# Kernel optimization log

Measured on AMD Instinct MI355X. Metric: run time of the kernel, lower is better.

Reference implementation:

```python
import jax, jax.numpy as jnp
import numpy as np

NEG_SLOPE = 0.2  # PyG GATConv default
BN_EPS = 1e-5
NUM_GRAPHS = 128


def _bn(x, g, b, m, v):
    # eval-mode BatchNorm1d with running stats
    return (x - m) * jax.lax.rsqrt(v + BN_EPS) * g + b


def _gat_conv(x, src, dst, mask, W, a_src, a_dst, bias):
    # PyG GATConv: per-head linear, edge logits LeakyReLU(a_src.Wx_j + a_dst.Wx_i),
    # segment-softmax over incoming edges of each dst node, scatter-add messages.
    N = x.shape[0]
    H, C = a_src.shape
    xw = (x @ W).reshape(N, H, C)                       # [N,H,C]
    logit_s = (xw * a_src).sum(-1)                      # [N,H]
    logit_d = (xw * a_dst).sum(-1)                      # [N,H]
    e = jax.nn.leaky_relu(logit_s[src] + logit_d[dst], NEG_SLOPE)  # [E,H]
    e = jnp.where(mask[:, None], e, -1e30)              # edges filtered by edge_weights==1
    m = jax.ops.segment_max(e, dst, num_segments=N)     # [N,H]
    m = jnp.maximum(m, -1e30)                           # guard empty segments
    p = jnp.exp(e - m[dst]) * mask[:, None].astype(e.dtype)
    denom = jax.ops.segment_sum(p, dst, num_segments=N) + 1e-16
    alpha = p / denom[dst]                              # [E,H]
    out = jax.ops.segment_sum(xw[src] * alpha[..., None], dst, num_segments=N)
    return out.reshape(N, H * C) + bias


def setup_inputs() -> dict:
    key = jax.random.key(0)
    ks = jax.random.split(key, 20)
    N, E, F, G, NC = 20000, 320000, 128, NUM_GRAPHS, 10
    E0, E1, H = 256, 512, 2
    C = E1 // H

    def lin(k, fi, fo):
        return jax.random.normal(k, (fi, fo), jnp.float32) / np.float32(np.sqrt(fi))

    def bn(k, n):
        k1, k2, k3, k4 = jax.random.split(k, 4)
        g = 1.0 + 0.1 * jax.random.normal(k1, (n,), jnp.float32)
        b = 0.1 * jax.random.normal(k2, (n,), jnp.float32)
        m = 0.1 * jax.random.normal(k3, (n,), jnp.float32)
        v = 1.0 + 0.5 * jax.random.uniform(k4, (n,), jnp.float32)
        return g, b, m, v

    d = {}
    d['x'] = jax.random.normal(ks[0], (N, F), jnp.float32)
    d['edge_index'] = jax.random.randint(ks[1], (2, E), 0, N, dtype=jnp.int32)
    d['edge_weights'] = jnp.ones((E,), jnp.int32)
    d['batch'] = jnp.sort(jax.random.randint(ks[2], (N,), 0, G, dtype=jnp.int32))
    d['mlp_w1'] = lin(ks[3], F, E0); d['mlp_b1'] = jnp.zeros((E0,), jnp.float32)
    d['bn1_g'], d['bn1_b'], d['bn1_m'], d['bn1_v'] = bn(ks[4], E0)
    d['mlp_w2'] = lin(ks[5], E0, E0); d['mlp_b2'] = jnp.zeros((E0,), jnp.float32)
    d['bn2_g'], d['bn2_b'], d['bn2_m'], d['bn2_v'] = bn(ks[6], E0)
    d['gat0_w'] = lin(ks[7], E0, H * C)
    d['gat0_asrc'] = 0.1 * jax.random.normal(ks[8], (H, C), jnp.float32)
    d['gat0_adst'] = 0.1 * jax.random.normal(ks[9], (H, C), jnp.float32)
    d['gat0_bias'] = jnp.zeros((H * C,), jnp.float32)
    d['gat1_w'] = lin(ks[10], E1, H * C)
    d['gat1_asrc'] = 0.1 * jax.random.normal(ks[11], (H, C), jnp.float32)
    d['gat1_adst'] = 0.1 * jax.random.normal(ks[12], (H, C), jnp.float32)
    d['gat1_bias'] = jnp.zeros((H * C,), jnp.float32)
    d['bn3_g'], d['bn3_b'], d['bn3_m'], d['bn3_v'] = bn(ks[13], E1)
    d['fin_w1'] = lin(ks[14], E1, E1); d['fin_b1'] = jnp.zeros((E1,), jnp.float32)
    d['fin_w2'] = lin(ks[15], E1, NC); d['fin_b2'] = jnp.zeros((NC,), jnp.float32)
    return d


def reference(x, edge_index, edge_weights, batch,
              mlp_w1, mlp_b1, bn1_g, bn1_b, bn1_m, bn1_v,
              mlp_w2, mlp_b2, bn2_g, bn2_b, bn2_m, bn2_v,
              gat0_w, gat0_asrc, gat0_adst, gat0_bias,
              gat1_w, gat1_asrc, gat1_adst, gat1_bias,
              bn3_g, bn3_b, bn3_m, bn3_v,
              fin_w1, fin_b1, fin_w2, fin_b2):
    src, dst = edge_index[0], edge_index[1]
    mask = edge_weights == 1
    # initial MLP (dropout is identity in eval)
    h = jax.nn.relu(_bn(x @ mlp_w1 + mlp_b1, bn1_g, bn1_b, bn1_m, bn1_v))
    h = jax.nn.relu(_bn(h @ mlp_w2 + mlp_b2, bn2_g, bn2_b, bn2_m, bn2_v))
    # GAT layers
    h = _gat_conv(h, src, dst, mask, gat0_w, gat0_asrc, gat0_adst, gat0_bias)
    h = _gat_conv(h, src, dst, mask, gat1_w, gat1_asrc, gat1_adst, gat1_bias)
    # global mean pool over graphs
    sums = jax.ops.segment_sum(h, batch, num_segments=NUM_GRAPHS)
    cnt = jax.ops.segment_sum(jnp.ones((h.shape[0], 1), h.dtype), batch, num_segments=NUM_GRAPHS)
    pooled = sums / jnp.maximum(cnt, 1.0)
    # final head: BN -> ReLU -> Linear -> ReLU -> Linear
    z = jax.nn.relu(_bn(pooled, bn3_g, bn3_b, bn3_m, bn3_v))
    z = jax.nn.relu(z @ fin_w1 + fin_b1)
    return z @ fin_w2 + fin_b2
```

## Files before the change

kernel.cpp:

```cpp
#include <hip/hip_runtime.h>

typedef unsigned short u16;

constexpr int NN = 20000;
constexpr int EE = 320000;
constexpr int FD = 128;
constexpr int C0 = 256;
constexpr int C1 = 512;
constexpr int NG = 128;
constexpr int NC = 10;
constexpr int NBLK = (NN + 255) / 256;
constexpr int HB  = 320;
constexpr int EST = HB * 256;
constexpr int LGB = 640;
constexpr int PSPL = 16;

constexpr size_t OFF_XB   = 0;
constexpr size_t OFF_H1   = OFF_XB  + (size_t)NN * FD * 2;
constexpr size_t OFF_H2   = OFF_H1  + (size_t)NN * C0 * 2;
constexpr size_t OFF_XW   = OFF_H2  + (size_t)NN * C0 * 2;
constexpr size_t OFF_H34  = OFF_XW  + (size_t)NN * C1 * 2;
constexpr size_t OFF_LS   = OFF_H34 + (size_t)NN * C1 * 2;
constexpr size_t OFF_LD   = OFF_LS  + (size_t)NN * 2 * 4;
constexpr size_t OFF_DEG  = OFF_LD  + (size_t)NN * 2 * 4;
constexpr size_t OFF_OFFS = OFF_DEG + (size_t)NN * 4;
constexpr size_t OFF_CUR  = OFF_OFFS + 80016;
constexpr size_t OFF_CSRC = OFF_CUR + (size_t)NN * 4;
constexpr size_t OFF_GCNT = OFF_CSRC + (size_t)EE * 4;
constexpr size_t OFF_GOFF = OFF_GCNT + 512;
constexpr size_t OFF_PART = OFF_GOFF + 768;
constexpr size_t OFF_PTOT = OFF_PART + 512;
constexpr size_t OFF_Z1   = OFF_PTOT + 256;
constexpr size_t OFF_Z2   = OFF_Z1  + (size_t)NG * C1 * 2;
constexpr size_t OFF_ST   = OFF_Z2  + (size_t)NG * C1 * 2;
constexpr size_t OFF_W1T  = OFF_ST  + 8192;
constexpr size_t OFF_W2T  = OFF_W1T + (size_t)FD * C0 * 2;
constexpr size_t OFF_G0T  = OFF_W2T + (size_t)C0 * C0 * 2;
constexpr size_t OFF_G1T  = OFF_G0T + (size_t)C0 * C1 * 2;
constexpr size_t OFF_AUX  = OFF_G1T + (size_t)C1 * C1 * 2;
constexpr size_t OFF_FLAG = OFF_AUX  + 0;
constexpr size_t OFF_A0S  = OFF_AUX  + 256;
constexpr size_t OFF_A0D  = OFF_AUX  + 1280;
constexpr size_t OFF_A1S  = OFF_AUX  + 2304;
constexpr size_t OFF_A1D  = OFF_AUX  + 3328;
constexpr size_t OFF_GB0  = OFF_AUX  + 4352;
constexpr size_t OFF_GB1  = OFF_AUX  + 6400;
constexpr size_t OFF_FB1  = OFF_AUX  + 8448;
constexpr size_t OFF_FB2  = OFF_AUX  + 10496;
constexpr size_t OFF_GMX  = OFF_AUX  + 10752;
constexpr size_t OFF_PP   = OFF_AUX  + 11008;
constexpr size_t OFF_P0   = OFF_XB;
constexpr size_t OFF_P1   = OFF_XB + (size_t)EE * 4;

__device__ inline float bf2f(u16 u) { return __uint_as_float(((unsigned)u) << 16); }
__device__ inline u16 f2bf(float f) {
    unsigned u = __float_as_uint(f);
    unsigned r = u + 0x7fffu + ((u >> 16) & 1u);
    return (u16)(r >> 16);
}
__device__ inline float ldf(const void* p, long i, unsigned f) {
    return f ? ((const float*)p)[i] : bf2f(((const u16*)p)[i]);
}
__device__ inline unsigned encf(float f) {
    unsigned u = __float_as_uint(f);
    return (u & 0x80000000u) ? ~u : (u | 0x80000000u);
}
__device__ inline float decf(unsigned e) {
    return (e & 0x80000000u) ? __uint_as_float(e ^ 0x80000000u) : __uint_as_float(~e);
}
__device__ inline void unpack8(uint4 r, float* v) {
    v[0] = __uint_as_float(r.x << 16); v[1] = __uint_as_float(r.x & 0xffff0000u);
    v[2] = __uint_as_float(r.y << 16); v[3] = __uint_as_float(r.y & 0xffff0000u);
    v[4] = __uint_as_float(r.z << 16); v[5] = __uint_as_float(r.z & 0xffff0000u);
    v[6] = __uint_as_float(r.w << 16); v[7] = __uint_as_float(r.w & 0xffff0000u);
}

typedef __bf16 bf16x8_t __attribute__((ext_vector_type(8)));
typedef float  f32x4_t  __attribute__((ext_vector_type(4)));

__device__ __forceinline__ void gl_lds16(const u16* g, u16* l) {
    __builtin_amdgcn_global_load_lds((const __attribute__((address_space(1))) void*)g,
                                     (__attribute__((address_space(3))) void*)l, 16, 0, 0);
}

__global__ void detect_dtype(const u16* __restrict__ x, const u16* __restrict__ w,
                             const u16* __restrict__ fw, unsigned* flag) {
    __shared__ int cnt;
    if (threadIdx.x == 0) cnt = 0;
    __syncthreads();
    int c = 0;
    for (int i = threadIdx.x; i < 4096; i += 256) {
        c += (((x[i]  >> 7) & 0xFF) == 0xFF);
        c += (((w[i]  >> 7) & 0xFF) == 0xFF);
        c += (((fw[i] >> 7) & 0xFF) == 0xFF);
    }
    atomicAdd(&cnt, c);
    __syncthreads();
    if (threadIdx.x == 0) *flag = (cnt >= 2) ? 1u : 0u;
}

__global__ void cvt_x(const unsigned* __restrict__ flag, const void* __restrict__ xin,
                      u16* __restrict__ XB, int* __restrict__ deg, int* __restrict__ gcnt,
                      unsigned* __restrict__ gmxu) {
    int i = blockIdx.x * 256 + threadIdx.x;
    if (i < NN) deg[i] = 0;
    if (i < NG) gcnt[i] = 0;
    if (i < 4)  gmxu[i] = encf(-1e30f);
    if (*flag) {
        float4 v = ((const float4*)xin)[i];
        ushort4 r;
        r.x = f2bf(v.x); r.y = f2bf(v.y); r.z = f2bf(v.z); r.w = f2bf(v.w);
        ((ushort4*)XB)[i] = r;
    } else {
        ((ushort4*)XB)[i] = ((const ushort4*)xin)[i];
    }
}

__global__ void prep_params(const unsigned* __restrict__ flag,
                            const void* g1, const void* b1, const void* m1, const void* v1, const void* lb1,
                            const void* g2, const void* b2, const void* m2, const void* v2, const void* lb2,
                            const void* g3, const void* b3, const void* m3, const void* v3,
                            const void* a0s, const void* a0d, const void* gb0in,
                            const void* a1s, const void* a1d, const void* gb1in,
                            const void* fb1in, const void* fb2in,
                            float* S1, float* T1, float* S2, float* T2, float* S3, float* T3,
                            u16* A0S, u16* A0D, u16* A1S, u16* A1D,
                            float* GB0, float* GB1, float* FB1, float* FB2) {
    unsigned f = *flag;
    int c = threadIdx.x;
    if (c < 256) {
        float s = ldf(g1, c, f) / sqrtf(ldf(v1, c, f) + 1e-5f);
        S1[c] = s; T1[c] = s * (ldf(lb1, c, f) - ldf(m1, c, f)) + ldf(b1, c, f);
        float s2 = ldf(g2, c, f) / sqrtf(ldf(v2, c, f) + 1e-5f);
        S2[c] = s2; T2[c] = s2 * (ldf(lb2, c, f) - ldf(m2, c, f)) + ldf(b2, c, f);
    }
    float s3 = ldf(g3, c, f) / sqrtf(ldf(v3, c, f) + 1e-5f);
    S3[c] = s3; T3[c] = ldf(b3, c, f) - ldf(m3, c, f) * s3;
    A0S[c] = f2bf(ldf(a0s, c, f));
    A0D[c] = f2bf(ldf(a0d, c, f));
    A1S[c] = f2bf(ldf(a1s, c, f));
    A1D[c] = f2bf(ldf(a1d, c, f));
    GB0[c] = ldf(gb0in, c, f);
    GB1[c] = ldf(gb1in, c, f);
    FB1[c] = ldf(fb1in, c, f);
    if (c < NC) FB2[c] = ldf(fb2in, c, f);
}

__global__ void transpose_all(const unsigned* __restrict__ flag,
                              const void* __restrict__ w1, const void* __restrict__ w2,
                              const void* __restrict__ g0, const void* __restrict__ g1,
                              u16* __restrict__ w1T, u16* __restrict__ w2T,
                              u16* __restrict__ g0T, u16* __restrict__ g1T) {
    int b = blockIdx.x;
    const void* B; u16* BT; int K, logN, base;
    if (b < 128)      { B = w1; BT = w1T; K = FD; logN = 8; base = 0; }
    else if (b < 384) { B = w2; BT = w2T; K = C0; logN = 8; base = 128; }
    else if (b < 896) { B = g0; BT = g0T; K = C0; logN = 9; base = 384; }
    else              { B = g1; BT = g1T; K = C1; logN = 9; base = 896; }
    int idx = (b - base) * 256 + threadIdx.x;
    int N = 1 << logN;
    int k = idx >> logN, n = idx & (N - 1);
    u16 v = (*flag) ? f2bf(((const float*)B)[idx]) : ((const u16*)B)[idx];
    BT[(size_t)n * K + k] = v;
}

__global__ __launch_bounds__(256) void hist_k(const int* __restrict__ dst, const int* __restrict__ ew,
                                              const int* __restrict__ batch,
                                              int* __restrict__ deg, int* __restrict__ gcnt) {
    int tid = blockIdx.x * 256 + threadIdx.x;
    int lane = threadIdx.x & 63;
#pragma unroll
    for (int j = 0; j < 4; j++) {
        int e = tid + j * EST;
        if (e < EE && ew[e] == 1) atomicAdd(&deg[dst[e]], 1);
    }
    int n = tid;
    if (n < NN) {
        int g = batch[n];
        int pg = __shfl_up(g, 1);
        bool head = (lane == 0) || (pg != g);
        unsigned long long act = __ballot(1);
        unsigned long long hm  = __ballot(head);
        if (head) {
            unsigned long long above = (lane < 63) ? ((hm >> (lane + 1)) << (lane + 1)) : 0ull;
            int limit = 64 - __builtin_clzll(act);
            int nxt = above ? __builtin_ctzll(above) : limit;
            atomicAdd(&gcnt[g], nxt - lane);
        }
    }
}
__global__ __launch_bounds__(256) void scan_blk(const int* __restrict__ deg, int* __restrict__ off,
                                                int* __restrict__ part) {
    __shared__ int tmp[256];
    int tid = threadIdx.x, i = blockIdx.x * 256 + tid;
    int v = (i < NN) ? deg[i] : 0;
    tmp[tid] = v;
    __syncthreads();
#pragma unroll
    for (int s = 1; s < 256; s <<= 1) {
        int a = (tid >= s) ? tmp[tid - s] : 0;
        __syncthreads();
        if (tid >= s) tmp[tid] += a;
        __syncthreads();
    }
    if (i < NN) off[i] = tmp[tid] - v;
    if (tid == 255) part[blockIdx.x] = tmp[255];
}
__global__ __launch_bounds__(128) void scan_small(int* __restrict__ part, int* __restrict__ ptot,
                                                  const int* __restrict__ gcnt, int* __restrict__ goff) {
    __shared__ int tmp[128];
    int tid = threadIdx.x;
    int v = (tid < NBLK) ? part[tid] : 0;
    tmp[tid] = v;
    __syncthreads();
#pragma unroll
    for (int s = 1; s < 128; s <<= 1) {
        int a = (tid >= s) ? tmp[tid - s] : 0;
        __syncthreads();
        if (tid >= s) tmp[tid] += a;
        __syncthreads();
    }
    if (tid < NBLK) part[tid] = tmp[tid] - v;
    if (tid == 127) *ptot = tmp[127];
    __syncthreads();
    int g = gcnt[tid];
    tmp[tid] = g;
    __syncthreads();
#pragma unroll
    for (int s = 1; s < 128; s <<= 1) {
        int a = (tid >= s) ? tmp[tid - s] : 0;
        __syncthreads();
        if (tid >= s) tmp[tid] += a;
        __syncthreads();
    }
    goff[tid] = tmp[tid] - g;
    if (tid == 127) goff[128] = tmp[127];
}
__global__ __launch_bounds__(256) void scan_add(int* __restrict__ off, const int* __restrict__ part,
                                                const int* __restrict__ ptot, int* __restrict__ cursor) {
    int tid = threadIdx.x, i = blockIdx.x * 256 + tid;
    if (i < NN) {
        int o = off[i] + part[blockIdx.x];
        off[i] = o;
        cursor[i] = o;
    }
    if (i == 0) off[NN] = *ptot;
}
__global__ __launch_bounds__(256) void csr_fill(const int* __restrict__ src, const int* __restrict__ dst,
                                                const int* __restrict__ ew,
                                                int* __restrict__ cursor, u16* __restrict__ csrc) {
    int tid = blockIdx.x * 256 + threadIdx.x;
    bool ok[4]; int sv[4]; int p[4];
#pragma unroll
    for (int j = 0; j < 4; j++) {
        int e = tid + j * EST;
        ok[j] = false; sv[j] = 0; p[j] = 0;
        if (e < EE && ew[e] == 1) {
            ok[j] = true;
            sv[j] = src[e];
            p[j] = atomicAdd(&cursor[dst[e]], 1);
        }
    }
#pragma unroll
    for (int j = 0; j < 4; j++) if (ok[j]) csrc[p[j]] = (u16)sv[j];
}

template <int EPI>
__global__ __launch_bounds__(256) void gemm_tile(const u16* __restrict__ A, const u16* __restrict__ BT,
                                                 u16* __restrict__ Cm,
                                                 const float* __restrict__ S, const float* __restrict__ T,
                                                 int M, int N, int K) {
    __shared__ u16 As[128 * 32];
    __shared__ u16 Bs[128 * 32];
    const int tid  = threadIdx.x;
    const int wave = tid >> 6;
    const int lane = tid & 63;
    const int quad = lane >> 4;
    const int l16  = lane & 15;
    const int wr0  = (wave >> 1) * 64;
    const int wc0  = (wave & 1) * 64;
    const int row0 = blockIdx.x * 128;
    const int col0 = blockIdx.y * 128;

    const int lr = lane >> 2;
    const int lk = (lane & 3) * 8;
    int r0l = wave * 32 + lr;
    int r1l = r0l + 16;
    int gr0 = row0 + r0l; if (gr0 >= M) gr0 = M - 1;
    int gr1 = row0 + r1l; if (gr1 >= M) gr1 = M - 1;
    const u16* ga0 = A  + (size_t)gr0 * K + lk;
    const u16* ga1 = A  + (size_t)gr1 * K + lk;
    const u16* gb0 = BT + (size_t)(col0 + r0l) * K + lk;
    const u16* gb1 = BT + (size_t)(col0 + r1l) * K + lk;
    u16* la0 = As + (size_t)(wave * 32)      * 32 + lane * 8;
    u16* la1 = As + (size_t)(wave * 32 + 16) * 32 + lane * 8;
    u16* lb0 = Bs + (size_t)(wave * 32)      * 32 + lane * 8;
    u16* lb1 = Bs + (size_t)(wave * 32 + 16) * 32 + lane * 8;

    f32x4_t acc[4][4];
#pragma unroll
    for (int r = 0; r < 4; r++)
#pragma unroll
        for (int c = 0; c < 4; c++)
#pragma unroll
            for (int i = 0; i < 4; i++) acc[r][c][i] = 0.f;

    for (int k0 = 0; k0 < K; k0 += 32) {
        gl_lds16(ga0 + k0, la0);
        gl_lds16(ga1 + k0, la1);
        gl_lds16(gb0 + k0, lb0);
        gl_lds16(gb1 + k0, lb1);
        __syncthreads();

        bf16x8_t a[4], b[4];
#pragma unroll
        for (int r = 0; r < 4; r++)
            a[r] = *(const bf16x8_t*)(As + (size_t)(wr0 + r * 16 + l16) * 32 + quad * 8);
#pragma unroll
        for (int c = 0; c < 4; c++)
            b[c] = *(const bf16x8_t*)(Bs + (size_t)(wc0 + c * 16 + l16) * 32 + quad * 8);
#pragma unroll
        for (int r = 0; r < 4; r++)
#pragma unroll
            for (int c = 0; c < 4; c++)
                acc[r][c] = __builtin_amdgcn_mfma_f32_16x16x32_bf16(a[r], b[c], acc[r][c], 0, 0, 0);
        __syncthreads();
    }

#pragma unroll
    for (int r = 0; r < 4; r++) {
        int rb = row0 + wr0 + r * 16 + quad * 4;
#pragma unroll
        for (int c = 0; c < 4; c++) {
            int col = col0 + wc0 + c * 16 + l16;
            float sc = (EPI == 1) ? S[col] : 0.f;
            float sh = (EPI == 1) ? T[col] : 0.f;
#pragma unroll
            for (int i = 0; i < 4; i++) {
                int row = rb + i;
                if (row < M) {
                    float v = acc[r][c][i];
                    if (EPI == 1) v = fmaxf(v * sc + sh, 0.f);
                    Cm[(size_t)row * N + col] = f2bf(v);
                }
            }
        }
    }
}

__global__ __launch_bounds__(256) void gat_logits(const u16* __restrict__ xw, const u16* __restrict__ asrc,
                                                  const u16* __restrict__ adst, float* __restrict__ ls,
                                                  float* __restrict__ ld, unsigned* __restrict__ gmx) {
    __shared__ float smax[8];
    int lane = threadIdx.x & 63;
    int wv   = threadIdx.x >> 6;
    int h    = lane >> 5;
    uint4 av = ((const uint4*)asrc)[lane];
    uint4 dv = ((const uint4*)adst)[lane];
    float a[8], d[8];
    unpack8(av, a); unpack8(dv, d);
    float mm = -1e30f;
    int n = blockIdx.x * 4 + wv;
    uint4 xv;
    if (n < NN) xv = ((const uint4*)(xw + (size_t)n * C1))[lane];
    while (n < NN) {
        int n2 = n + LGB * 4;
        uint4 nx;
        if (n2 < NN) nx = ((const uint4*)(xw + (size_t)n2 * C1))[lane];
        float x[8];
        unpack8(xv, x);
        float ps = 0.f, pd = 0.f;
#pragma unroll
        for (int j = 0; j < 8; j++) { ps += x[j] * a[j]; pd += x[j] * d[j]; }
#pragma unroll
        for (int m = 16; m >= 1; m >>= 1) { ps += __shfl_xor(ps, m); pd += __shfl_xor(pd, m); }
        if ((lane & 31) == 0) {
            ls[n * 2 + h] = ps;
            ld[n * 2 + h] = pd;
        }
        mm = fmaxf(mm, ps);
        xv = nx; n = n2;
    }
    if ((lane & 31) == 0) smax[wv * 2 + h] = mm;
    __syncthreads();
    if (threadIdx.x < 2) {
        float m = fmaxf(fmaxf(smax[threadIdx.x], smax[2 + threadIdx.x]),
                        fmaxf(smax[4 + threadIdx.x], smax[6 + threadIdx.x]));
        atomicMax(&gmx[threadIdx.x], encf(m));
    }
}

__global__ __launch_bounds__(256) void gat_prep(const int* __restrict__ off, const u16* __restrict__ csrc,
                                                const float* __restrict__ ls, const float* __restrict__ ld,
                                                const unsigned* __restrict__ gmx,
                                                float* __restrict__ P0, float* __restrict__ P1) {
    int n = blockIdx.x * 4 + (threadIdx.x >> 6);
    if (n >= NN) return;
    int lane = threadIdx.x & 63;
    int h = lane >> 5;
    int el = lane & 31;
    int beg = off[n], end = off[n + 1];
    if (beg >= end) return;
    float2 ldv = ((const float2*)ld)[n];
    float ldh = h ? ldv.y : ldv.x;
    float gm = decf(gmx[h]) + ldh;
    float mhat = gm > 0.f ? gm : 0.2f * gm;
    float* __restrict__ Ph = h ? P1 : P0;
    float den = 0.f;
    for (int base = beg; base < end; base += 32) {
        int e = base + el;
        int ec = e < end ? e : end - 1;
        int sv = csrc[ec];
        float vv = ls[sv * 2 + h] + ldh;
        vv = vv > 0.f ? vv : 0.2f * vv;
        float p = __expf(vv - mhat);
        float pm = (e < end) ? p : 0.f;
#pragma unroll
        for (int m = 16; m >= 1; m >>= 1) pm += __shfl_xor(pm, m);
        den += pm;
        if (e < end) Ph[e] = p;
    }
    float inv = 1.f / fmaxf(den, 1e-30f);
    for (int base = beg; base < end; base += 32) {
        int e = base + el;
        if (e < end) Ph[e] *= inv;
    }
}

__device__ __forceinline__ void proc_edge(uint4 c, float w, float* acc) {
    float x[8];
    unpack8(c, x);
#pragma unroll
    for (int q = 0; q < 8; q++) acc[q] = fmaf(w, x[q], acc[q]);
}

__global__ __launch_bounds__(256) void gat_aggregate(const int* __restrict__ off, const u16* __restrict__ csrc,
                                                     const float* __restrict__ P0, const float* __restrict__ P1,
                                                     const u16* __restrict__ xw,
                                                     const float* __restrict__ bias, u16* __restrict__ outh) {
    int n = blockIdx.x * 4 + (threadIdx.x >> 6);
    if (n >= NN) return;
    const int lane = threadIdx.x & 63;
    const int h    = lane >> 5;
    const int el   = lane & 31;
    const int hoff = h << 5;
    const float* __restrict__ Ph = h ? P1 : P0;
    int beg = off[n], end = off[n + 1];

    float acc[8];
#pragma unroll
    for (int q = 0; q < 8; q++) acc[q] = 0.f;

#define ROWLD(S) (((const uint4*)(xw + (size_t)(S) * C1))[lane])

    for (int base = beg; base < end; base += 32) {
        int cnt = end - base; if (cnt > 32) cnt = 32;
        int e = base + el;
        int ec = e < end ? e : end - 1;
        int sv = csrc[ec];
        float pv = Ph[ec];

        uint4 r0 = ROWLD(__shfl(sv, 0));
        uint4 r1 = ROWLD(__shfl(sv, 1));
        uint4 r2 = ROWLD(__shfl(sv, 2));
        uint4 r3 = ROWLD(__shfl(sv, 3));

        for (int j = 0; j < cnt; j += 4) {
            uint4 c0 = r0, c1 = r1, c2 = r2, c3 = r3;
            float w0 = __shfl(pv, j + hoff);
            float w1 = __shfl(pv, j + 1 + hoff);
            float w2 = __shfl(pv, j + 2 + hoff);
            float w3 = __shfl(pv, j + 3 + hoff);
            if (j + 4 < cnt) {
                r0 = ROWLD(__shfl(sv, j + 4));
                r1 = ROWLD(__shfl(sv, j + 5));
                r2 = ROWLD(__shfl(sv, j + 6));
                r3 = ROWLD(__shfl(sv, j + 7));
            }
            proc_edge(c0, w0, acc);
            if (j + 1 < cnt) proc_edge(c1, w1, acc);
            if (j + 2 < cnt) proc_edge(c2, w2, acc);
            if (j + 3 < cnt) proc_edge(c3, w3, acc);
        }
    }
#undef ROWLD

    int cb = lane * 8;
    const float4* bp = (const float4*)(bias + cb);
    float4 b0 = bp[0], b1 = bp[1];
    uint4 st;
    st.x = (unsigned)f2bf(acc[0] + b0.x) | ((unsigned)f2bf(acc[1] + b0.y) << 16);
    st.y = (unsigned)f2bf(acc[2] + b0.z) | ((unsigned)f2bf(acc[3] + b0.w) << 16);
    st.z = (unsigned)f2bf(acc[4] + b1.x) | ((unsigned)f2bf(acc[5] + b1.y) << 16);
    st.w = (unsigned)f2bf(acc[6] + b1.z) | ((unsigned)f2bf(acc[7] + b1.w) << 16);
    ((uint4*)(outh + (size_t)n * C1 + cb))[0] = st;
}

__global__ __launch_bounds__(128) void pool_part(const u16* __restrict__ h4, const int* __restrict__ goff,
                                                 float* __restrict__ pp) {
    int g = blockIdx.x, s = blockIdx.y, t = threadIdx.x;
    int b = goff[g], e = goff[g + 1];
    int len = e - b;
    int chunk = (len + PSPL - 1) / PSPL;
    int n0 = b + s * chunk;
    int n1 = n0 + chunk; if (n1 > e) n1 = e;
    float s0 = 0.f, s1 = 0.f, s2 = 0.f, s3 = 0.f;
    for (int n = n0; n < n1; n++) {
        ushort4 v = *(const ushort4*)(h4 + (size_t)n * C1 + t * 4);
        s0 += bf2f(v.x); s1 += bf2f(v.y); s2 += bf2f(v.z); s3 += bf2f(v.w);
    }
    float4* dst = (float4*)(pp + ((size_t)g * PSPL + s) * C1 + t * 4);
    *dst = make_float4(s0, s1, s2, s3);
}

__global__ __launch_bounds__(512) void pool_fin(const float* __restrict__ pp, const int* __restrict__ goff,
                                                const float* __restrict__ S3, const float* __restrict__ T3,
                                                u16* __restrict__ z1) {
    int g = blockIdx.x, t = threadIdx.x;
    float s = 0.f;
#pragma unroll
    for (int k = 0; k < PSPL; k++) s += pp[((size_t)g * PSPL + k) * C1 + t];
    int b = goff[g], e = goff[g + 1];
    float mean = s / fmaxf((float)(e - b), 1.f);
    float v = mean * S3[t] + T3[t];
    z1[(size_t)g * C1 + t] = f2bf(fmaxf(v, 0.f));
}

__global__ __launch_bounds__(512) void head_fc1(const unsigned* __restrict__ flag, const u16* __restrict__ z1,
                                                const void* __restrict__ w1, const float* __restrict__ FB1,
                                                u16* __restrict__ z2) {
    __shared__ float zrow[512];
    int g = blockIdx.x, t = threadIdx.x;
    zrow[t] = bf2f(z1[(size_t)g * 512 + t]);
    __syncthreads();
    float acc = 0.f;
    if (*flag) {
        const float* w = (const float*)w1;
        for (int k = 0; k < 512; k++) acc = fmaf(zrow[k], w[(size_t)k * 512 + t], acc);
    } else {
        const u16* w = (const u16*)w1;
        for (int k = 0; k < 512; k++) acc = fmaf(zrow[k], bf2f(w[(size_t)k * 512 + t]), acc);
    }
    acc += FB1[t];
    z2[(size_t)g * 512 + t] = f2bf(fmaxf(acc, 0.f));
}
__global__ __launch_bounds__(64) void head_fc2(const unsigned* __restrict__ flag, const u16* __restrict__ z2,
                                               const void* __restrict__ w2, const float* __restrict__ FB2,
                                               void* __restrict__ out) {
    int g = blockIdx.x, o = blockIdx.y, lane = threadIdx.x;
    unsigned f = *flag;
    float acc = 0.f;
    if (f) {
        const float* w = (const float*)w2;
        for (int k = lane; k < 512; k += 64) acc += bf2f(z2[(size_t)g * 512 + k]) * w[(size_t)k * NC + o];
    } else {
        const u16* w = (const u16*)w2;
        for (int k = lane; k < 512; k += 64) acc += bf2f(z2[(size_t)g * 512 + k]) * bf2f(w[(size_t)k * NC + o]);
    }
#pragma unroll
    for (int m = 32; m >= 1; m >>= 1) acc += __shfl_xor(acc, m);
    if (lane == 0) {
        float v = acc + FB2[o];
        if (f) ((float*)out)[g * NC + o] = v;
        else   ((u16*)out)[g * NC + o] = f2bf(v);
    }
}

extern "C" void kernel_launch(void* const* d_in, const int* in_sizes, int n_in,
                              void* d_out, int out_size, void* d_ws, size_t ws_size,
                              hipStream_t stream) {
    (void)in_sizes; (void)n_in; (void)out_size; (void)ws_size;

    const void* x      = d_in[0];
    const int* ei      = (const int*)d_in[1];
    const int* src     = ei;
    const int* dst     = ei + EE;
    const int* ew      = (const int*)d_in[2];
    const int* batch   = (const int*)d_in[3];
    const void* mlp_w1 = d_in[4];
    const void* mlp_b1 = d_in[5];
    const void *bn1g = d_in[6], *bn1b = d_in[7], *bn1m = d_in[8], *bn1v = d_in[9];
    const void* mlp_w2 = d_in[10];
    const void* mlp_b2 = d_in[11];
    const void *bn2g = d_in[12], *bn2b = d_in[13], *bn2m = d_in[14], *bn2v = d_in[15];
    const void* g0w    = d_in[16];
    const void* g0as   = d_in[17];
    const void* g0ad   = d_in[18];
    const void* g0bias = d_in[19];
    const void* g1w    = d_in[20];
    const void* g1as   = d_in[21];
    const void* g1ad   = d_in[22];
    const void* g1bias = d_in[23];
    const void *bn3g = d_in[24], *bn3b = d_in[25], *bn3m = d_in[26], *bn3v = d_in[27];
    const void* fin_w1 = d_in[28];
    const void* fin_b1 = d_in[29];
    const void* fin_w2 = d_in[30];
    const void* fin_b2 = d_in[31];

    char* ws = (char*)d_ws;
    u16*  XB   = (u16*)(ws + OFF_XB);
    u16*  h1   = (u16*)(ws + OFF_H1);
    u16*  h2   = (u16*)(ws + OFF_H2);
    u16*  xw   = (u16*)(ws + OFF_XW);
    u16*  h34  = (u16*)(ws + OFF_H34);
    float* ls  = (float*)(ws + OFF_LS);
    float* ld  = (float*)(ws + OFF_LD);
    int*  deg  = (int*)(ws + OFF_DEG);
    int*  off  = (int*)(ws + OFF_OFFS);
    int*  cur  = (int*)(ws + OFF_CUR);
    u16*  csrc = (u16*)(ws + OFF_CSRC);
    int*  gcnt = (int*)(ws + OFF_GCNT);
    int*  goff = (int*)(ws + OFF_GOFF);
    int*  part = (int*)(ws + OFF_PART);
    int*  ptot = (int*)(ws + OFF_PTOT);
    u16*  z1   = (u16*)(ws + OFF_Z1);
    u16*  z2   = (u16*)(ws + OFF_Z2);
    float* S1 = (float*)(ws + OFF_ST);
    float* T1 = S1 + 256;
    float* S2 = T1 + 256;
    float* T2 = S2 + 256;
    float* S3 = T2 + 256;
    float* T3 = S3 + 512;
    u16* w1T = (u16*)(ws + OFF_W1T);
    u16* w2T = (u16*)(ws + OFF_W2T);
    u16* g0T = (u16*)(ws + OFF_G0T);
    u16* g1T = (u16*)(ws + OFF_G1T);
    unsigned* flag = (unsigned*)(ws + OFF_FLAG);
    u16* A0S = (u16*)(ws + OFF_A0S);
    u16* A0D = (u16*)(ws + OFF_A0D);
    u16* A1S = (u16*)(ws + OFF_A1S);
    u16* A1D = (u16*)(ws + OFF_A1D);
    float* GB0 = (float*)(ws + OFF_GB0);
    float* GB1 = (float*)(ws + OFF_GB1);
    float* FB1 = (float*)(ws + OFF_FB1);
    float* FB2 = (float*)(ws + OFF_FB2);
    unsigned* GMXU = (unsigned*)(ws + OFF_GMX);
    float* PP = (float*)(ws + OFF_PP);
    float* P0 = (float*)(ws + OFF_P0);
    float* P1 = (float*)(ws + OFF_P1);

    detect_dtype<<<1, 256, 0, stream>>>((const u16*)x, (const u16*)mlp_w1, (const u16*)fin_w1, flag);
    cvt_x<<<(NN * FD / 4) / 256, 256, 0, stream>>>(flag, x, XB, deg, gcnt, GMXU);
    prep_params<<<1, 512, 0, stream>>>(flag,
                                       bn1g, bn1b, bn1m, bn1v, mlp_b1,
                                       bn2g, bn2b, bn2m, bn2v, mlp_b2,
                                       bn3g, bn3b, bn3m, bn3v,
                                       g0as, g0ad, g0bias, g1as, g1ad, g1bias,
                                       fin_b1, fin_b2,
                                       S1, T1, S2, T2, S3, T3,
                                       A0S, A0D, A1S, A1D, GB0, GB1, FB1, FB2);
    transpose_all<<<1920, 256, 0, stream>>>(flag, mlp_w1, mlp_w2, g0w, g1w, w1T, w2T, g0T, g1T);

    hist_k<<<HB, 256, 0, stream>>>(dst, ew, batch, deg, gcnt);
    scan_blk<<<NBLK, 256, 0, stream>>>(deg, off, part);
    scan_small<<<1, 128, 0, stream>>>(part, ptot, gcnt, goff);
    scan_add<<<NBLK, 256, 0, stream>>>(off, part, ptot, cur);
    csr_fill<<<HB, 256, 0, stream>>>(src, dst, ew, cur, csrc);

    gemm_tile<1><<<dim3(157, 2), 256, 0, stream>>>(XB, w1T, h1, S1, T1, NN, C0, FD);
    gemm_tile<1><<<dim3(157, 2), 256, 0, stream>>>(h1, w2T, h2, S2, T2, NN, C0, C0);

    gemm_tile<0><<<dim3(157, 4), 256, 0, stream>>>(h2, g0T, xw, nullptr, nullptr, NN, C1, C0);
    gat_logits<<<LGB, 256, 0, stream>>>(xw, A0S, A0D, ls, ld, GMXU);
    gat_prep<<<NN / 4, 256, 0, stream>>>(off, csrc, ls, ld, GMXU, P0, P1);
    gat_aggregate<<<NN / 4, 256, 0, stream>>>(off, csrc, P0, P1, xw, GB0, h34);

    gemm_tile<0><<<dim3(157, 4), 256, 0, stream>>>(h34, g1T, xw, nullptr, nullptr, NN, C1, C1);
    gat_logits<<<LGB, 256, 0, stream>>>(xw, A1S, A1D, ls, ld, GMXU + 2);
    gat_prep<<<NN / 4, 256, 0, stream>>>(off, csrc, ls, ld, GMXU + 2, P0, P1);
    gat_aggregate<<<NN / 4, 256, 0, stream>>>(off, csrc, P0, P1, xw, GB1, h34);

    pool_part<<<dim3(NG, PSPL), 128, 0, stream>>>(h34, goff, PP);
    pool_fin<<<NG, 512, 0, stream>>>(PP, goff, S3, T3, z1);
    head_fc1<<<NG, 512, 0, stream>>>(flag, z1, fin_w1, FB1, z2);
    head_fc2<<<dim3(NG, NC), 64, 0, stream>>>(flag, z2, fin_w2, FB2, d_out);
}
```

Measured before the change: 407.1 us.

## Fuse param prep with transposes, defer softmax normalization, merge head kernels

Merges the parameter-prep and weight-transpose kernels into one launch, and combines pool_fin, head_fc1 and head_fc2 into a single head kernel. GAT prep no longer rescales the per-edge probabilities in a second pass. It stores each node's denominator, and the aggregate kernel multiplies its accumulator by the reciprocal in the epilogue. This removes several launches and one read-write pass over the edge weights, at the cost of an extra small buffer and a serial shared-memory reduction for the final layer.

After: 405.7 us. About the same (-0.4%).

```diff
diff --git a/kernel.cpp b/kernel.cpp
--- a/kernel.cpp
+++ b/kernel.cpp
@@ -49,6 +49,7 @@
 constexpr size_t OFF_FB2  = OFF_AUX  + 10496;
 constexpr size_t OFF_GMX  = OFF_AUX  + 10752;
 constexpr size_t OFF_PP   = OFF_AUX  + 11008;
+constexpr size_t OFF_DENA = OFF_PP + (size_t)NG * PSPL * C1 * 4;
 constexpr size_t OFF_P0   = OFF_XB;
 constexpr size_t OFF_P1   = OFF_XB + (size_t)EE * 4;
 
@@ -116,7 +117,7 @@
     }
 }
 
-__global__ void prep_params(const unsigned* __restrict__ flag,
+__global__ __launch_bounds__(512) void prep_trans(const unsigned* __restrict__ flag,
                             const void* g1, const void* b1, const void* m1, const void* v1, const void* lb1,
                             const void* g2, const void* b2, const void* m2, const void* v2, const void* lb2,
                             const void* g3, const void* b3, const void* m3, const void* v3,
@@ -125,42 +126,40 @@
                             const void* fb1in, const void* fb2in,
                             float* S1, float* T1, float* S2, float* T2, float* S3, float* T3,
                             u16* A0S, u16* A0D, u16* A1S, u16* A1D,
-                            float* GB0, float* GB1, float* FB1, float* FB2) {
+                            float* GB0, float* GB1, float* FB1, float* FB2,
+                            const void* w1, const void* w2, const void* g0w, const void* g1w,
+                            u16* w1T, u16* w2T, u16* g0T, u16* g1T) {
     unsigned f = *flag;
-    int c = threadIdx.x;
-    if (c < 256) {
-        float s = ldf(g1, c, f) / sqrtf(ldf(v1, c, f) + 1e-5f);
-        S1[c] = s; T1[c] = s * (ldf(lb1, c, f) - ldf(m1, c, f)) + ldf(b1, c, f);
-        float s2 = ldf(g2, c, f) / sqrtf(ldf(v2, c, f) + 1e-5f);
-        S2[c] = s2; T2[c] = s2 * (ldf(lb2, c, f) - ldf(m2, c, f)) + ldf(b2, c, f);
-    }
-    float s3 = ldf(g3, c, f) / sqrtf(ldf(v3, c, f) + 1e-5f);
-    S3[c] = s3; T3[c] = ldf(b3, c, f) - ldf(m3, c, f) * s3;
-    A0S[c] = f2bf(ldf(a0s, c, f));
-    A0D[c] = f2bf(ldf(a0d, c, f));
-    A1S[c] = f2bf(ldf(a1s, c, f));
-    A1D[c] = f2bf(ldf(a1d, c, f));
-    GB0[c] = ldf(gb0in, c, f);
-    GB1[c] = ldf(gb1in, c, f);
-    FB1[c] = ldf(fb1in, c, f);
-    if (c < NC) FB2[c] = ldf(fb2in, c, f);
-}
-
-__global__ void transpose_all(const unsigned* __restrict__ flag,
-                              const void* __restrict__ w1, const void* __restrict__ w2,
-                              const void* __restrict__ g0, const void* __restrict__ g1,
-                              u16* __restrict__ w1T, u16* __restrict__ w2T,
-                              u16* __restrict__ g0T, u16* __restrict__ g1T) {
-    int b = blockIdx.x;
+    if (blockIdx.x == 0) {
+        int c = threadIdx.x;
+        if (c < 256) {
+            float s = ldf(g1, c, f) / sqrtf(ldf(v1, c, f) + 1e-5f);
+            S1[c] = s; T1[c] = s * (ldf(lb1, c, f) - ldf(m1, c, f)) + ldf(b1, c, f);
+            float s2 = ldf(g2, c, f) / sqrtf(ldf(v2, c, f) + 1e-5f);
+            S2[c] = s2; T2[c] = s2 * (ldf(lb2, c, f) - ldf(m2, c, f)) + ldf(b2, c, f);
+        }
+        float s3 = ldf(g3, c, f) / sqrtf(ldf(v3, c, f) + 1e-5f);
+        S3[c] = s3; T3[c] = ldf(b3, c, f) - ldf(m3, c, f) * s3;
+        A0S[c] = f2bf(ldf(a0s, c, f));
+        A0D[c] = f2bf(ldf(a0d, c, f));
+        A1S[c] = f2bf(ldf(a1s, c, f));
+        A1D[c] = f2bf(ldf(a1d, c, f));
+        GB0[c] = ldf(gb0in, c, f);
+        GB1[c] = ldf(gb1in, c, f);
+        FB1[c] = ldf(fb1in, c, f);
+        if (c < NC) FB2[c] = ldf(fb2in, c, f);
+        return;
+    }
+    int b = blockIdx.x - 1;
     const void* B; u16* BT; int K, logN, base;
-    if (b < 128)      { B = w1; BT = w1T; K = FD; logN = 8; base = 0; }
-    else if (b < 384) { B = w2; BT = w2T; K = C0; logN = 8; base = 128; }
-    else if (b < 896) { B = g0; BT = g0T; K = C0; logN = 9; base = 384; }
-    else              { B = g1; BT = g1T; K = C1; logN = 9; base = 896; }
-    int idx = (b - base) * 256 + threadIdx.x;
+    if (b < 64)       { B = w1;  BT = w1T; K = FD; logN = 8; base = 0; }
+    else if (b < 192) { B = w2;  BT = w2T; K = C0; logN = 8; base = 64; }
+    else if (b < 448) { B = g0w; BT = g0T; K = C0; logN = 9; base = 192; }
+    else              { B = g1w; BT = g1T; K = C1; logN = 9; base = 448; }
+    int idx = (b - base) * 512 + threadIdx.x;
     int N = 1 << logN;
     int k = idx >> logN, n = idx & (N - 1);
-    u16 v = (*flag) ? f2bf(((const float*)B)[idx]) : ((const u16*)B)[idx];
+    u16 v = f ? f2bf(((const float*)B)[idx]) : ((const u16*)B)[idx];
     BT[(size_t)n * K + k] = v;
 }
 
@@ -393,14 +392,14 @@
 __global__ __launch_bounds__(256) void gat_prep(const int* __restrict__ off, const u16* __restrict__ csrc,
                                                 const float* __restrict__ ls, const float* __restrict__ ld,
                                                 const unsigned* __restrict__ gmx,
-                                                float* __restrict__ P0, float* __restrict__ P1) {
+                                                float* __restrict__ P0, float* __restrict__ P1,
+                                                float* __restrict__ denA) {
     int n = blockIdx.x * 4 + (threadIdx.x >> 6);
     if (n >= NN) return;
     int lane = threadIdx.x & 63;
     int h = lane >> 5;
     int el = lane & 31;
     int beg = off[n], end = off[n + 1];
-    if (beg >= end) return;
     float2 ldv = ((const float2*)ld)[n];
     float ldh = h ? ldv.y : ldv.x;
     float gm = decf(gmx[h]) + ldh;
@@ -420,11 +419,7 @@
         den += pm;
         if (e < end) Ph[e] = p;
     }
-    float inv = 1.f / fmaxf(den, 1e-30f);
-    for (int base = beg; base < end; base += 32) {
-        int e = base + el;
-        if (e < end) Ph[e] *= inv;
-    }
+    if (el == 0) denA[n * 2 + h] = den;
 }
 
 __device__ __forceinline__ void proc_edge(uint4 c, float w, float* acc) {
@@ -436,6 +431,7 @@
 
 __global__ __launch_bounds__(256) void gat_aggregate(const int* __restrict__ off, const u16* __restrict__ csrc,
                                                      const float* __restrict__ P0, const float* __restrict__ P1,
+                                                     const float* __restrict__ denA,
                                                      const u16* __restrict__ xw,
                                                      const float* __restrict__ bias, u16* __restrict__ outh) {
     int n = blockIdx.x * 4 + (threadIdx.x >> 6);
@@ -485,14 +481,15 @@
     }
 #undef ROWLD
 
+    float inv = 1.f / fmaxf(denA[n * 2 + h], 1e-30f);
     int cb = lane * 8;
     const float4* bp = (const float4*)(bias + cb);
     float4 b0 = bp[0], b1 = bp[1];
     uint4 st;
-    st.x = (unsigned)f2bf(acc[0] + b0.x) | ((unsigned)f2bf(acc[1] + b0.y) << 16);
-    st.y = (unsigned)f2bf(acc[2] + b0.z) | ((unsigned)f2bf(acc[3] + b0.w) << 16);
-    st.z = (unsigned)f2bf(acc[4] + b1.x) | ((unsigned)f2bf(acc[5] + b1.y) << 16);
-    st.w = (unsigned)f2bf(acc[6] + b1.z) | ((unsigned)f2bf(acc[7] + b1.w) << 16);
+    st.x = (unsigned)f2bf(fmaf(acc[0], inv, b0.x)) | ((unsigned)f2bf(fmaf(acc[1], inv, b0.y)) << 16);
+    st.y = (unsigned)f2bf(fmaf(acc[2], inv, b0.z)) | ((unsigned)f2bf(fmaf(acc[3], inv, b0.w)) << 16);
+    st.z = (unsigned)f2bf(fmaf(acc[4], inv, b1.x)) | ((unsigned)f2bf(fmaf(acc[5], inv, b1.y)) << 16);
+    st.w = (unsigned)f2bf(fmaf(acc[6], inv, b1.z)) | ((unsigned)f2bf(fmaf(acc[7], inv, b1.w)) << 16);
     ((uint4*)(outh + (size_t)n * C1 + cb))[0] = st;
 }
 
@@ -513,28 +510,27 @@
     *dst = make_float4(s0, s1, s2, s3);
 }
 
-__global__ __launch_bounds__(512) void pool_fin(const float* __restrict__ pp, const int* __restrict__ goff,
+__global__ __launch_bounds__(512) void head_all(const unsigned* __restrict__ flag,
+                                                const float* __restrict__ pp, const int* __restrict__ goff,
                                                 const float* __restrict__ S3, const float* __restrict__ T3,
-                                                u16* __restrict__ z1) {
+                                                const void* __restrict__ w1, const float* __restrict__ FB1,
+                                                const void* __restrict__ w2, const float* __restrict__ FB2,
+                                                void* __restrict__ out) {
+    __shared__ float zrow[512];
+    __shared__ float z2row[512];
+    __shared__ float red[512];
     int g = blockIdx.x, t = threadIdx.x;
+    unsigned f = *flag;
     float s = 0.f;
 #pragma unroll
     for (int k = 0; k < PSPL; k++) s += pp[((size_t)g * PSPL + k) * C1 + t];
     int b = goff[g], e = goff[g + 1];
     float mean = s / fmaxf((float)(e - b), 1.f);
-    float v = mean * S3[t] + T3[t];
-    z1[(size_t)g * C1 + t] = f2bf(fmaxf(v, 0.f));
-}
-
-__global__ __launch_bounds__(512) void head_fc1(const unsigned* __restrict__ flag, const u16* __restrict__ z1,
-                                                const void* __restrict__ w1, const float* __restrict__ FB1,
-                                                u16* __restrict__ z2) {
-    __shared__ float zrow[512];
-    int g = blockIdx.x, t = threadIdx.x;
-    zrow[t] = bf2f(z1[(size_t)g * 512 + t]);
+    float v = fmaxf(mean * S3[t] + T3[t], 0.f);
+    zrow[t] = bf2f(f2bf(v));
     __syncthreads();
     float acc = 0.f;
-    if (*flag) {
+    if (f) {
         const float* w = (const float*)w1;
         for (int k = 0; k < 512; k++) acc = fmaf(zrow[k], w[(size_t)k * 512 + t], acc);
     } else {
@@ -542,27 +538,25 @@
         for (int k = 0; k < 512; k++) acc = fmaf(zrow[k], bf2f(w[(size_t)k * 512 + t]), acc);
     }
     acc += FB1[t];
-    z2[(size_t)g * 512 + t] = f2bf(fmaxf(acc, 0.f));
-}
-__global__ __launch_bounds__(64) void head_fc2(const unsigned* __restrict__ flag, const u16* __restrict__ z2,
-                                               const void* __restrict__ w2, const float* __restrict__ FB2,
-                                               void* __restrict__ out) {
-    int g = blockIdx.x, o = blockIdx.y, lane = threadIdx.x;
-    unsigned f = *flag;
-    float acc = 0.f;
-    if (f) {
-        const float* w = (const float*)w2;
-        for (int k = lane; k < 512; k += 64) acc += bf2f(z2[(size_t)g * 512 + k]) * w[(size_t)k * NC + o];
-    } else {
-        const u16* w = (const u16*)w2;
-        for (int k = lane; k < 512; k += 64) acc += bf2f(z2[(size_t)g * 512 + k]) * bf2f(w[(size_t)k * NC + o]);
-    }
-#pragma unroll
-    for (int m = 32; m >= 1; m >>= 1) acc += __shfl_xor(acc, m);
-    if (lane == 0) {
-        float v = acc + FB2[o];
-        if (f) ((float*)out)[g * NC + o] = v;
-        else   ((u16*)out)[g * NC + o] = f2bf(v);
+    z2row[t] = bf2f(f2bf(fmaxf(acc, 0.f)));
+    __syncthreads();
+    float z2t = z2row[t];
+    for (int o = 0; o < NC; o++) {
+        float p = f ? z2t * ((const float*)w2)[(size_t)t * NC + o]
+                    : z2t * bf2f(((const u16*)w2)[(size_t)t * NC + o]);
+        red[t] = p;
+        __syncthreads();
+#pragma unroll
+        for (int sd = 256; sd >= 1; sd >>= 1) {
+            if (t < sd) red[t] += red[t + sd];
+            __syncthreads();
+        }
+        if (t == 0) {
+            float vv = red[0] + FB2[o];
+            if (f) ((float*)out)[g * NC + o] = vv;
+            else   ((u16*)out)[g * NC + o] = f2bf(vv);
+        }
+        __syncthreads();
     }
 }
 
@@ -613,8 +607,6 @@
     int*  goff = (int*)(ws + OFF_GOFF);
     int*  part = (int*)(ws + OFF_PART);
     int*  ptot = (int*)(ws + OFF_PTOT);
-    u16*  z1   = (u16*)(ws + OFF_Z1);
-    u16*  z2   = (u16*)(ws + OFF_Z2);
     float* S1 = (float*)(ws + OFF_ST);
     float* T1 = S1 + 256;
     float* S2 = T1 + 256;
@@ -636,20 +628,21 @@
     float* FB2 = (float*)(ws + OFF_FB2);
     unsigned* GMXU = (unsigned*)(ws + OFF_GMX);
     float* PP = (float*)(ws + OFF_PP);
+    float* DENA = (float*)(ws + OFF_DENA);
     float* P0 = (float*)(ws + OFF_P0);
     float* P1 = (float*)(ws + OFF_P1);
 
     detect_dtype<<<1, 256, 0, stream>>>((const u16*)x, (const u16*)mlp_w1, (const u16*)fin_w1, flag);
     cvt_x<<<(NN * FD / 4) / 256, 256, 0, stream>>>(flag, x, XB, deg, gcnt, GMXU);
-    prep_params<<<1, 512, 0, stream>>>(flag,
-                                       bn1g, bn1b, bn1m, bn1v, mlp_b1,
-                                       bn2g, bn2b, bn2m, bn2v, mlp_b2,
-                                       bn3g, bn3b, bn3m, bn3v,
-                                       g0as, g0ad, g0bias, g1as, g1ad, g1bias,
-                                       fin_b1, fin_b2,
-                                       S1, T1, S2, T2, S3, T3,
-                                       A0S, A0D, A1S, A1D, GB0, GB1, FB1, FB2);
-    transpose_all<<<1920, 256, 0, stream>>>(flag, mlp_w1, mlp_w2, g0w, g1w, w1T, w2T, g0T, g1T);
+    prep_trans<<<961, 512, 0, stream>>>(flag,
+                                        bn1g, bn1b, bn1m, bn1v, mlp_b1,
+                                        bn2g, bn2b, bn2m, bn2v, mlp_b2,
+                                        bn3g, bn3b, bn3m, bn3v,
+                                        g0as, g0ad, g0bias, g1as, g1ad, g1bias,
+                                        fin_b1, fin_b2,
+                                        S1, T1, S2, T2, S3, T3,
+                                        A0S, A0D, A1S, A1D, GB0, GB1, FB1, FB2,
+                                        mlp_w1, mlp_w2, g0w, g1w, w1T, w2T, g0T, g1T);
 
     hist_k<<<HB, 256, 0, stream>>>(dst, ew, batch, deg, gcnt);
     scan_blk<<<NBLK, 256, 0, stream>>>(deg, off, part);
@@ -662,16 +655,14 @@
 
     gemm_tile<0><<<dim3(157, 4), 256, 0, stream>>>(h2, g0T, xw, nullptr, nullptr, NN, C1, C0);
     gat_logits<<<LGB, 256, 0, stream>>>(xw, A0S, A0D, ls, ld, GMXU);
-    gat_prep<<<NN / 4, 256, 0, stream>>>(off, csrc, ls, ld, GMXU, P0, P1);
-    gat_aggregate<<<NN / 4, 256, 0, stream>>>(off, csrc, P0, P1, xw, GB0, h34);
+    gat_prep<<<NN / 4, 256, 0, stream>>>(off, csrc, ls, ld, GMXU, P0, P1, DENA);
+    gat_aggregate<<<NN / 4, 256, 0, stream>>>(off, csrc, P0, P1, DENA, xw, GB0, h34);
 
     gemm_tile<0><<<dim3(157, 4), 256, 0, stream>>>(h34, g1T, xw, nullptr, nullptr, NN, C1, C1);
     gat_logits<<<LGB, 256, 0, stream>>>(xw, A1S, A1D, ls, ld, GMXU + 2);
-    gat_prep<<<NN / 4, 256, 0, stream>>>(off, csrc, ls, ld, GMXU + 2, P0, P1);
-    gat_aggregate<<<NN / 4, 256, 0, stream>>>(off, csrc, P0, P1, xw, GB1, h34);
+    gat_prep<<<NN / 4, 256, 0, stream>>>(off, csrc, ls, ld, GMXU + 2, P0, P1, DENA);
+    gat_aggregate<<<NN / 4, 256, 0, stream>>>(off, csrc, P0, P1, DENA, xw, GB1, h34);
 
     pool_part<<<dim3(NG, PSPL), 128, 0, stream>>>(h34, goff, PP);
-    pool_fin<<<NG, 512, 0, stream>>>(PP, goff, S3, T3, z1);
-    head_fc1<<<NG, 512, 0, stream>>>(flag, z1, fin_w1, FB1, z2);
-    head_fc2<<<dim3(NG, NC), 64, 0, stream>>>(flag, z2, fin_w2, FB2, d_out);
-}
+    head_all<<<NG, 512, 0, stream>>>(flag, PP, goff, S3, T3, fin_w1, FB1, fin_w2, FB2, d_out);
+}
```
